# Performance work log

Hardware: AMD Instinct MI355X
Metric: run time of the kernel (lower is better)

Reference implementation:

```python
import jax, jax.numpy as jnp
import numpy as np

_J6 = jnp.array([[0,0,0,0,0,1],[0,0,0,0,-1,0],[0,0,0,1,0,0],
                 [0,0,1,0,0,0],[0,-1,0,0,0,0],[1,0,0,0,0,0]], dtype=jnp.float32)
_PAIRS4 = [(0,1),(0,2),(0,3),(1,2),(1,3),(2,3)]  # combinations(range(4),2)


def exterior(p1, p2):
    # Plucker line coords of two 4-vectors, normalized. (...,4)x(...,4)->(...,6)
    parts = [p1[..., i] * p2[..., j] - p1[..., j] * p2[..., i] for i, j in _PAIRS4]
    L = jnp.stack(parts, axis=-1)
    n = jnp.maximum(jnp.linalg.norm(L, axis=-1, keepdims=True), 1e-12)
    return L / n


def setup_inputs() -> dict:
    key = jax.random.key(0)
    B, T, D, H = 2, 2048, 1024, 16
    ks = jax.random.split(key, 10)
    w = lambda k, shape: jax.random.normal(k, shape, jnp.float32) * 0.02
    return {
        "x": jax.random.normal(ks[0], (B, T, D), jnp.float32),
        "qkv_w": w(ks[1], (3 * D, D)),
        "qkv_b": jnp.zeros((3 * D,), jnp.float32),
        "w1w": w(ks[2], (4 * H, D)),
        "w2w": w(ks[3], (4 * H, D)),
        "r1w": w(ks[4], (4 * H, D)),
        "r2w": w(ks[5], (4 * H, D)),
        "memv_w": w(ks[6], (D, D)),
        "memv_b": jnp.zeros((D,), jnp.float32),
        "memg_w": w(ks[7], (H, D)),
        "memg_b": jnp.zeros((H,), jnp.float32),
        "mem_scale": jnp.full((H,), 0.1, jnp.float32),
        "iter_mix": jnp.array(0.0, jnp.float32),
        "out_w": w(ks[8], (D, D)),
        "out_b": jnp.zeros((D,), jnp.float32),
        "decay_logits": jnp.full((H,), 4.6, jnp.float32),
    }


def reference(x, qkv_w, qkv_b, w1w, w2w, r1w, r2w, memv_w, memv_b,
              memg_w, memg_b, mem_scale, iter_mix, out_w, out_b, decay_logits):
    B, T, D = x.shape
    H = decay_logits.shape[0]
    dh = D // H
    pd = 6
    scale = dh ** -0.5

    # --- standard causal softmax attention ---
    qkv = (x @ qkv_w.T + qkv_b).reshape(B, T, 3, H, dh)
    qkv = jnp.transpose(qkv, (2, 0, 3, 1, 4))  # (3,B,H,T,dh)
    q, k, v = qkv[0], qkv[1], qkv[2]
    scores = jnp.einsum('bhtd,bhsd->bhts', q, k) * scale
    causal = jnp.triu(jnp.ones((T, T), dtype=bool), 1)
    scores = jnp.where(causal, -jnp.inf, scores)
    attn = jax.nn.softmax(scores, axis=-1)  # dropout is identity in eval
    seq_out = jnp.einsum('bhts,bhsd->bhtd', attn, v)
    seq_out = jnp.transpose(seq_out, (0, 2, 1, 3)).reshape(B, T, D)

    # --- decay-weighted Gram memory (linear-attention style state) ---
    x_prev = jnp.concatenate([jnp.zeros((B, 1, D), x.dtype), x[:, :-1]], axis=1)
    w1 = (x_prev @ w1w.T).reshape(B, T, H, 4)
    w2 = (x @ w2w.T).reshape(B, T, H, 4)
    write_lines = exterior(w1, w2)  # (B,T,H,6)
    r1 = (x @ r1w.T).reshape(B, T, H, 4)
    r2 = (x @ r2w.T).reshape(B, T, H, 4)
    read_lines = exterior(r1, r2)

    Jw = jnp.einsum('bthi,ij->bhtj', write_lines, _J6)  # (B,H,T,6)
    rd = jnp.transpose(read_lines, (0, 2, 1, 3))        # (B,H,T,6)

    decays = jax.nn.sigmoid(decay_logits)               # (H,)
    pos = jnp.arange(T, dtype=x.dtype)
    outer = Jw[..., :, None] * Jw[..., None, :]         # (B,H,T,6,6)
    decay_inv = (1.0 / jnp.maximum(decays, 1e-6))[:, None] ** pos[None, :]  # (H,T)
    outer_scaled = outer * decay_inv[None, :, :, None, None]
    M_cumsum = jnp.cumsum(outer_scaled, axis=2)
    M_cumsum = jnp.concatenate(
        [jnp.zeros((B, H, 1, pd, pd), x.dtype), M_cumsum[:, :, :-1]], axis=2)
    decay_fwd = decays[:, None] ** pos[None, :]
    M_all = M_cumsum * decay_fwd[None, :, :, None, None]

    rd_M = jnp.einsum('bhti,bhtij->bhtj', rd, M_all)
    score_M = jnp.sum(rd_M * rd, axis=-1)    # (B,H,T)
    score_M2 = jnp.sum(rd_M * rd_M, axis=-1)
    alpha = jax.nn.sigmoid(iter_mix)
    mem_score = (1 - alpha) * score_M + alpha * score_M2

    mem_val = x @ memv_w.T + memv_b                     # (B,T,D)
    gate = jax.nn.sigmoid(x @ memg_w.T + memg_b)        # (B,T,H)
    mem_score_t = jnp.transpose(mem_score, (0, 2, 1))   # (B,T,H)
    gated = jax.nn.sigmoid(mem_score_t * mem_scale) * gate
    gated = jnp.mean(gated, axis=-1, keepdims=True)     # (B,T,1)

    return (seq_out + gated * mem_val) @ out_w.T + out_b
```

## Files before the change

kernel.cpp:

```cpp
#include <hip/hip_runtime.h>
#include <stdint.h>

#define TT 2048
#define DD 1024
#define HH 16
#define LDP 4368
#define SCH 64
#define SNC (TT/SCH)

using bf16x8 = __attribute__((ext_vector_type(8))) __bf16;
using u16x8  = __attribute__((ext_vector_type(8))) unsigned short;
using f32x4  = __attribute__((ext_vector_type(4))) float;

__device__ __forceinline__ float bf2f(unsigned short u){
  unsigned int x = ((unsigned int)u) << 16;
  return __builtin_bit_cast(float, x);
}
__device__ __forceinline__ unsigned short f2bf(float f){
  unsigned int x = __builtin_bit_cast(unsigned int, f);
  x += 0x7fffu + ((x >> 16) & 1u);
  return (unsigned short)(x >> 16);
}
__device__ __forceinline__ float sigmoidf_(float x){ return 1.0f/(1.0f+__expf(-x)); }

__device__ __forceinline__ void gload_lds16(const void* g, void* l){
  auto gp = (const __attribute__((address_space(1))) unsigned int*)(uintptr_t)g;
  auto lp = (__attribute__((address_space(3))) unsigned int*)(unsigned int)(uintptr_t)l;
  __builtin_amdgcn_global_load_lds(gp, lp, 16, 0, 0);
}

__global__ void prep_all_kernel(const float* __restrict__ qkv_w, const float* __restrict__ w1w,
                                const float* __restrict__ w2w, const float* __restrict__ r1w,
                                const float* __restrict__ r2w, const float* __restrict__ memv_w,
                                const float* __restrict__ memg_w, const float* __restrict__ out_w,
                                const float* __restrict__ qkv_b, const float* __restrict__ memv_b,
                                const float* __restrict__ memg_b, const float* __restrict__ x,
                                unsigned short* __restrict__ Wcat, float* __restrict__ bcat,
                                unsigned short* __restrict__ xb)
{
  const int blk = blockIdx.x;
  if (blk < 5392) {
    const int idx = blk*256 + threadIdx.x;
    {
      const int row = idx >> 8, c4 = (idx & 255)*4;
      const float* src; int r;
      if      (row < 3072) { src = qkv_w;  r = row; }
      else if (row < 3136) { src = w1w;    r = row-3072; }
      else if (row < 3200) { src = w2w;    r = row-3136; }
      else if (row < 3264) { src = r1w;    r = row-3200; }
      else if (row < 3328) { src = r2w;    r = row-3264; }
      else if (row < 4352) { src = memv_w; r = row-3328; }
      else if (row < 4368) { src = memg_w; r = row-4352; }
      else                 { src = out_w;  r = row-4368; }
      const float4 v = *(const float4*)(src + (size_t)r*1024 + c4);
      ushort4 o; o.x=f2bf(v.x); o.y=f2bf(v.y); o.z=f2bf(v.z); o.w=f2bf(v.w);
      *(ushort4*)(Wcat + (size_t)row*1024 + c4) = o;
    }
    if (idx < 4368) {
      float v;
      if      (idx < 3072) v = qkv_b[idx];
      else if (idx < 3328) v = 0.f;
      else if (idx < 4352) v = memv_b[idx-3328];
      else                 v = memg_b[idx-4352];
      bcat[idx] = v;
    }
  } else {
    const int idx = (blk - 5392)*256 + threadIdx.x;
    const float4 v = ((const float4*)x)[idx];
    ushort4 o; o.x=f2bf(v.x); o.y=f2bf(v.y); o.z=f2bf(v.z); o.w=f2bf(v.w);
    ((ushort4*)xb)[idx] = o;
  }
}

template<bool OUTF32>
__global__ __launch_bounds__(256, 3)
void gemm_bt_kernel(const unsigned short* __restrict__ A, int lda,
                    const unsigned short* __restrict__ Bt, int ldb,
                    const float* __restrict__ bias,
                    void* __restrict__ Cout, int ldc, int N, int K)
{
  __shared__ unsigned short smem[24576];
  const int tid = threadIdx.x;
  const int w = tid >> 6, lane = tid & 63;
  const int l15 = lane & 15, l4 = lane >> 4;
  const int m0 = blockIdx.x * 128;
  const int n0 = blockIdx.y * 128;
  const int wr = (w >> 1) * 64, wc = (w & 1) * 64;

  const f32x4 zero = {0.f,0.f,0.f,0.f};
  f32x4 acc[4][4];
#pragma unroll
  for (int i = 0; i < 4; ++i)
#pragma unroll
    for (int j = 0; j < 4; ++j) acc[i][j] = zero;

  const int srow = lane >> 2;
  const int k8   = (lane & 3) * 8;

  auto stage = [&](int k0, int buf) {
#pragma unroll
    for (int q = 0; q < 4; ++q) {
      const int c = q*4 + w;
      const int rloc = (c & 7)*16 + srow;
      if (c < 8) {
        gload_lds16(A + (size_t)(m0 + rloc)*lda + k0 + k8,
                    (char*)smem + buf*8192 + (c&7)*1024);
      } else {
        int nrow = n0 + rloc; if (nrow >= N) nrow = N - 1;
        gload_lds16(Bt + (size_t)nrow*ldb + k0 + k8,
                    (char*)smem + 24576 + buf*8192 + (c&7)*1024);
      }
    }
  };

  stage(0, 0);
  if (K > 32) stage(32, 1);

  int ti = 0;
  for (int k0 = 0; k0 < K; k0 += 32, ++ti) {
    if (k0 + 32 < K) { asm volatile("s_waitcnt vmcnt(4)" ::: "memory"); }
    else             { asm volatile("s_waitcnt vmcnt(0)" ::: "memory"); }
    __builtin_amdgcn_s_barrier();
    if (k0 + 64 < K) stage(k0 + 64, (ti + 2) % 3);

    const int cur = ti % 3;
    bf16x8 af[4], bfr[4];
#pragma unroll
    for (int i = 0; i < 4; ++i) {
      af[i]  = *reinterpret_cast<const bf16x8*>((const char*)smem + cur*8192
                 + (wr + i*16 + l15)*64 + l4*16);
      bfr[i] = *reinterpret_cast<const bf16x8*>((const char*)smem + 24576 + cur*8192
                 + (wc + i*16 + l15)*64 + l4*16);
    }
#pragma unroll
    for (int i = 0; i < 4; ++i)
#pragma unroll
      for (int j = 0; j < 4; ++j)
        acc[i][j] = __builtin_amdgcn_mfma_f32_16x16x32_bf16(af[i], bfr[j], acc[i][j], 0, 0, 0);
  }

  if (OUTF32) {
#pragma unroll
    for (int i = 0; i < 4; ++i) {
      const int rowb = m0 + wr + i*16 + l4*4;
#pragma unroll
      for (int j = 0; j < 4; ++j) {
        const int col = n0 + wc + j*16 + l15;
        if (col < N) {
          const float bv = bias ? bias[col] : 0.0f;
#pragma unroll
          for (int r = 0; r < 4; ++r)
            ((float*)Cout)[(size_t)(rowb + r)*ldc + col] = acc[i][j][r] + bv;
        }
      }
    }
  } else {
    __syncthreads();
#pragma unroll
    for (int i = 0; i < 4; ++i) {
      const int rloc = wr + i*16 + l4*4;
#pragma unroll
      for (int j = 0; j < 4; ++j) {
        const int col = wc + j*16 + l15;
        const float bv = bias ? bias[n0 + col] : 0.0f;
#pragma unroll
        for (int r = 0; r < 4; ++r)
          smem[(rloc + r)*128 + col] = f2bf(acc[i][j][r] + bv);
      }
    }
    __syncthreads();
#pragma unroll
    for (int p = 0; p < 8; ++p) {
      const int idx = p*256 + tid;
      const int row = idx >> 4;
      const int c8  = (idx & 15) * 8;
      if (n0 + c8 + 8 <= N) {
        *(u16x8*)((unsigned short*)Cout + (size_t)(m0 + row)*ldc + n0 + c8) =
            *(const u16x8*)&smem[row*128 + c8];
      }
    }
  }
}

__global__ __launch_bounds__(256, 4)
void transpose_v_kernel(const unsigned short* __restrict__ P, unsigned short* __restrict__ VT)
{
  __shared__ unsigned short tile[64][66];
  const int t0 = blockIdx.x*64, h = blockIdx.y, b = blockIdx.z;
  for (int i = threadIdx.x; i < 4096; i += 256) {
    const int r = i >> 6, c = i & 63;
    tile[r][c] = P[(size_t)(b*TT + t0 + r)*LDP + 2048 + h*64 + c];
  }
  __syncthreads();
  for (int i = threadIdx.x; i < 4096; i += 256) {
    const int d = i >> 6, tl = i & 63;
    VT[(size_t)((b*HH + h)*64 + d)*TT + t0 + tl] = tile[tl][d];
  }
}

__global__ __launch_bounds__(256, 2)
void attn_kernel(const unsigned short* __restrict__ P,
                 const unsigned short* __restrict__ VT,
                 float* __restrict__ seqo)
{
  __shared__ unsigned short Ks[2][128*64];
  __shared__ unsigned short Vs[2][64*128];
  __shared__ unsigned short Pls[4][16*128];

  const int tid = threadIdx.x;
  const int w = tid >> 6, lane = tid & 63;
  const int l15 = lane & 15, l4 = lane >> 4;
  const int pi = blockIdx.x, h = blockIdx.y, b = blockIdx.z;

  auto stage = [&](int kt, int bufsel) {
#pragma unroll
    for (int q2 = 0; q2 < 4; ++q2) {
      const int idx = q2*256 + tid;
      {
        const int r = idx >> 3;
        const int cb = ((idx & 7)*16) ^ ((r & 7) << 4);
        gload_lds16(P + (size_t)(b*TT + kt*128 + r)*LDP + 1024 + h*64 + (cb >> 1),
                    (char*)Ks[bufsel] + q2*4096 + w*1024);
      }
      {
        const int r = idx >> 4;
        const int cb = ((idx & 15)*16) ^ ((r & 7) << 4);
        gload_lds16(VT + (size_t)((b*HH + h)*64 + r)*TT + kt*128 + (cb >> 1),
                    (char*)Vs[bufsel] + q2*4096 + w*1024);
      }
    }
  };

  const f32x4 zero = {0.f,0.f,0.f,0.f};
  const unsigned xorb = ((unsigned)(l15 & 7u)) << 4;

  for (int rep = 0; rep < 2; ++rep) {
    const int qt = rep == 0 ? pi : 31 - pi;
    const int qbase = qt * 64;
    const int qrow = qbase + w*16 + l15;
    const int nt = (qt >> 1) + 1;

    bf16x8 qa[2];
    {
      const size_t base = (size_t)(b*TT + qbase + w*16 + l15)*LDP + h*64 + l4*8;
      qa[0] = *reinterpret_cast<const bf16x8*>(P + base);
      qa[1] = *reinterpret_cast<const bf16x8*>(P + base + 32);
    }

    f32x4 o[4];
#pragma unroll
    for (int d = 0; d < 4; ++d) o[d] = zero;
    float mrow = -1e30f;
    float lrow = 0.f;

    stage(0, 0);
    asm volatile("s_waitcnt vmcnt(0)" ::: "memory");
    __builtin_amdgcn_s_barrier();

    for (int kt = 0; kt < nt; ++kt) {
      const int cur = kt & 1;
      if (kt + 1 < nt) stage(kt + 1, cur ^ 1);

      f32x4 s[8];
#pragma unroll
      for (int kk = 0; kk < 8; ++kk) {
        f32x4 a = zero;
#pragma unroll
        for (int c = 0; c < 2; ++c) {
          const unsigned kbyte = (unsigned)((kk*16 + l15)*128)
                               + (((unsigned)(c*64 + l4*16)) ^ xorb);
          const bf16x8 kb = *reinterpret_cast<const bf16x8*>((const char*)Ks[cur] + kbyte);
          a = __builtin_amdgcn_mfma_f32_16x16x32_bf16(kb, qa[c], a, 0, 0, 0);
        }
        s[kk] = a;
      }

      if (kt == nt - 1) {
#pragma unroll
        for (int kk = 0; kk < 8; ++kk)
#pragma unroll
          for (int j = 0; j < 4; ++j) {
            const int kcol = kt*128 + kk*16 + l4*4 + j;
            s[kk][j] = (kcol <= qrow) ? s[kk][j]*0.125f : -1e30f;
          }
      } else {
#pragma unroll
        for (int kk = 0; kk < 8; ++kk)
#pragma unroll
          for (int j = 0; j < 4; ++j) s[kk][j] *= 0.125f;
      }

      float am[8];
#pragma unroll
      for (int kk = 0; kk < 8; ++kk)
        am[kk] = fmaxf(fmaxf(s[kk][0], s[kk][1]), fmaxf(s[kk][2], s[kk][3]));
      float tmax = fmaxf(fmaxf(fmaxf(am[0], am[1]), fmaxf(am[2], am[3])),
                         fmaxf(fmaxf(am[4], am[5]), fmaxf(am[6], am[7])));
      tmax = fmaxf(tmax, __shfl_xor(tmax, 16));
      tmax = fmaxf(tmax, __shfl_xor(tmax, 32));
      const float mn = fmaxf(mrow, tmax);
      const float corr = __expf(mrow - mn);
      mrow = mn;
      float lsum = 0.f;
#pragma unroll
      for (int kk = 0; kk < 8; ++kk) {
        float p0 = __expf(s[kk][0] - mn);
        float p1 = __expf(s[kk][1] - mn);
        float p2 = __expf(s[kk][2] - mn);
        float p3 = __expf(s[kk][3] - mn);
        s[kk][0] = p0; s[kk][1] = p1; s[kk][2] = p2; s[kk][3] = p3;
        lsum += (p0 + p1) + (p2 + p3);
      }
      lsum += __shfl_xor(lsum, 16);
      lsum += __shfl_xor(lsum, 32);
      lrow = lrow*corr + lsum;

      float corrq[4];
#pragma unroll
      for (int j = 0; j < 4; ++j) corrq[j] = __shfl(corr, l4*4 + j, 16);
#pragma unroll
      for (int d = 0; d < 4; ++d)
#pragma unroll
        for (int j = 0; j < 4; ++j) o[d][j] *= corrq[j];

      const unsigned pbase = (unsigned)(w*4096);
#pragma unroll
      for (int kk = 0; kk < 8; ++kk)
#pragma unroll
        for (int jp = 0; jp < 2; ++jp) {
          const unsigned v = (unsigned)f2bf(s[kk][jp*2]) | ((unsigned)f2bf(s[kk][jp*2+1]) << 16);
          const unsigned k = (unsigned)(kk*16 + l4*4 + jp*2);
          unsigned byte = (unsigned)l15*256u + ((k*2u) ^ xorb);
          *(unsigned*)((char*)Pls + pbase + byte) = v;
        }
      asm volatile("s_waitcnt lgkmcnt(0)" ::: "memory");

#pragma unroll
      for (int c = 0; c < 4; ++c) {
        const unsigned abyte = (unsigned)(l15*256) + (((unsigned)(c*64 + l4*16)) ^ xorb);
        const bf16x8 pa = *reinterpret_cast<const bf16x8*>((char*)Pls + pbase + abyte);
#pragma unroll
        for (int d = 0; d < 4; ++d) {
          const unsigned vbyte = (unsigned)((d*16 + l15)*256)
                               + (((unsigned)(c*64 + l4*16)) ^ xorb);
          const bf16x8 vb = *reinterpret_cast<const bf16x8*>((const char*)Vs[cur] + vbyte);
          o[d] = __builtin_amdgcn_mfma_f32_16x16x32_bf16(pa, vb, o[d], 0, 0, 0);
        }
      }

      asm volatile("s_waitcnt lgkmcnt(0)" ::: "memory");
      asm volatile("s_waitcnt vmcnt(0)" ::: "memory");
      __builtin_amdgcn_s_barrier();
    }

    float lrowq[4];
#pragma unroll
    for (int j = 0; j < 4; ++j) lrowq[j] = __shfl(lrow, l4*4 + j, 16);
#pragma unroll
    for (int d = 0; d < 4; ++d)
#pragma unroll
      for (int j = 0; j < 4; ++j) {
        const int row = qbase + w*16 + l4*4 + j;
        seqo[(size_t)(b*TT + row)*DD + h*64 + d*16 + l15] = o[d][j] / lrowq[j];
      }
  }
}

__device__ __forceinline__ void ext6(const float* p, const float* q, float* L){
  L[0] = p[0]*q[1] - p[1]*q[0];
  L[1] = p[0]*q[2] - p[2]*q[0];
  L[2] = p[0]*q[3] - p[3]*q[0];
  L[3] = p[1]*q[2] - p[2]*q[1];
  L[4] = p[1]*q[3] - p[3]*q[1];
  L[5] = p[2]*q[3] - p[3]*q[2];
  const float n2 = L[0]*L[0]+L[1]*L[1]+L[2]*L[2]+L[3]*L[3]+L[4]*L[4]+L[5]*L[5];
  const float inv = 1.0f / fmaxf(sqrtf(n2), 1e-12f);
#pragma unroll
  for (int i = 0; i < 6; ++i) L[i] *= inv;
}

__device__ __forceinline__ void load4bf(const unsigned short* p, float* o){
  const ushort4 u = *(const ushort4*)p;
  o[0] = bf2f(u.x); o[1] = bf2f(u.y); o[2] = bf2f(u.z); o[3] = bf2f(u.w);
}

__global__ __launch_bounds__(64, 8)
void scan_passA(const unsigned short* __restrict__ P, const float* __restrict__ decay_logits,
                float* __restrict__ E)
{
  __shared__ float jwS[SCH][6];
  const int bid = blockIdx.x;
  const int s = bid >> 5, c = bid & (SNC-1);
  const int b_ = s >> 4, h = s & (HH-1);
  const int lane = threadIdx.x;

  {
    const int t = c*SCH + lane;
    const size_t row = (size_t)(b_*TT + t)*LDP;
    float w1[4], w2[4];
    if (t > 0) load4bf(P + row - LDP + 3072 + h*4, w1);
    else { w1[0]=w1[1]=w1[2]=w1[3]=0.f; }
    load4bf(P + row + 3136 + h*4, w2);
    float wl[6];
    ext6(w1, w2, wl);
    jwS[lane][0]= wl[5]; jwS[lane][1]=-wl[4]; jwS[lane][2]= wl[3];
    jwS[lane][3]= wl[2]; jwS[lane][4]=-wl[1]; jwS[lane][5]= wl[0];
  }
  __syncthreads();

  const int i = lane & 7, j = lane >> 3;
  const int ic = i < 6 ? i : 0, jc = j < 6 ? j : 0;
  const float d = sigmoidf_(decay_logits[h]);
  float e = 0.f;
  for (int t = 0; t < SCH; ++t)
    e = d*(e + jwS[t][ic]*jwS[t][jc]);
  if (i < 6 && j < 6) E[(size_t)bid*36 + j*6 + i] = e;
}

__global__ __launch_bounds__(64, 8)
void scan_passC(const unsigned short* __restrict__ P, const float* __restrict__ E,
                const float* __restrict__ decay_logits,
                const float* __restrict__ iter_mix, float* __restrict__ msc)
{
  __shared__ float Ls[SCH][12];
  const int bid = blockIdx.x;
  const int s = bid >> 5, c = bid & (SNC-1);
  const int b_ = s >> 4, h = s & (HH-1);
  const int lane = threadIdx.x;

  {
    const int t = c*SCH + lane;
    const size_t row = (size_t)(b_*TT + t)*LDP;
    float w1[4], w2[4], r1[4], r2[4];
    if (t > 0) load4bf(P + row - LDP + 3072 + h*4, w1);
    else { w1[0]=w1[1]=w1[2]=w1[3]=0.f; }
    load4bf(P + row + 3136 + h*4, w2);
    load4bf(P + row + 3200 + h*4, r1);
    load4bf(P + row + 3264 + h*4, r2);
    float wl[6], rl[6];
    ext6(w1, w2, wl);
    ext6(r1, r2, rl);
    Ls[lane][0]= wl[5]; Ls[lane][1]=-wl[4]; Ls[lane][2]= wl[3];
    Ls[lane][3]= wl[2]; Ls[lane][4]=-wl[1]; Ls[lane][5]= wl[0];
#pragma unroll
    for (int q = 0; q < 6; ++q) Ls[lane][6+q] = rl[q];
  }
  __syncthreads();

  const int i = lane & 7, j = lane >> 3;
  const bool valid = (i < 6) && (j < 6);
  const int ic = i < 6 ? i : 0, jc = j < 6 ? j : 0;
  const float d = sigmoidf_(decay_logits[h]);
  const float alpha = sigmoidf_(iter_mix[0]);

  float m = 0.f;
  if (valid) {
    const float dL = __powf(d, (float)SCH);
    for (int cp = 0; cp < c; ++cp)
      m = dL*m + E[((size_t)s*SNC + cp)*36 + j*6 + i];
  }

  for (int t = 0; t < SCH; ++t) {
    const float ai = Ls[t][ic];
    const float aj = Ls[t][jc];
    const float ri = Ls[t][6+ic];
    const float rj = Ls[t][6+jc];
    float part = valid ? ri*m : 0.f;
    part += __shfl_xor(part, 1);
    part += __shfl_xor(part, 2);
    part += __shfl_xor(part, 4);
    float contrib = (i == 0 && j < 6) ? part*((1.f-alpha)*rj + alpha*part) : 0.f;
    contrib += __shfl_xor(contrib, 8);
    contrib += __shfl_xor(contrib, 16);
    contrib += __shfl_xor(contrib, 32);
    if (lane == 0) msc[((size_t)b_*TT + c*SCH + t)*HH + h] = contrib;
    m = d*(m + ai*aj);
  }
}

__global__ __launch_bounds__(256, 4)
void combine_kernel(const float* __restrict__ seqo, const unsigned short* __restrict__ P,
                    const float* __restrict__ msc, const float* __restrict__ mem_scale,
                    unsigned short* __restrict__ zb)
{
  const int w = threadIdx.x >> 6, lane = threadIdx.x & 63;
  const int row = blockIdx.x*4 + w;
  float val = 0.f;
  if (lane < HH) {
    const float ms = msc[(size_t)row*HH + lane];
    const float gl = bf2f(P[(size_t)row*LDP + 4352 + lane]);
    val = sigmoidf_(ms*mem_scale[lane]) * sigmoidf_(gl);
  }
  val += __shfl_xor(val, 1);
  val += __shfl_xor(val, 2);
  val += __shfl_xor(val, 4);
  val += __shfl_xor(val, 8);
  const float g = __shfl(val, 0) * (1.0f/16.0f);
#pragma unroll
  for (int it = 0; it < 4; ++it) {
    const int dcol = it*256 + lane*4;
    const float4 sv = *(const float4*)&seqo[(size_t)row*DD + dcol];
    const ushort4 pv = *(const ushort4*)&P[(size_t)row*LDP + 3328 + dcol];
    ushort4 o;
    o.x = f2bf(sv.x + g*bf2f(pv.x));
    o.y = f2bf(sv.y + g*bf2f(pv.y));
    o.z = f2bf(sv.z + g*bf2f(pv.z));
    o.w = f2bf(sv.w + g*bf2f(pv.w));
    *(ushort4*)&zb[(size_t)row*DD + dcol] = o;
  }
}

extern "C" void kernel_launch(void* const* d_in, const int* in_sizes, int n_in,
                              void* d_out, int out_size, void* d_ws, size_t ws_size,
                              hipStream_t stream)
{
  const float* x            = (const float*)d_in[0];
  const float* qkv_w        = (const float*)d_in[1];
  const float* qkv_b        = (const float*)d_in[2];
  const float* w1w          = (const float*)d_in[3];
  const float* w2w          = (const float*)d_in[4];
  const float* r1w          = (const float*)d_in[5];
  const float* r2w          = (const float*)d_in[6];
  const float* memv_w       = (const float*)d_in[7];
  const float* memv_b       = (const float*)d_in[8];
  const float* memg_w       = (const float*)d_in[9];
  const float* memg_b       = (const float*)d_in[10];
  const float* mem_scale    = (const float*)d_in[11];
  const float* iter_mix     = (const float*)d_in[12];
  const float* out_w        = (const float*)d_in[13];
  const float* out_b        = (const float*)d_in[14];
  const float* decay_logits = (const float*)d_in[15];

  char* ws = (char*)d_ws;
  unsigned short* xb   = (unsigned short*)(ws + 0);
  unsigned short* Wcat = (unsigned short*)(ws + 8388608);
  float*          bcat = (float*)         (ws + 19431424);
  unsigned short* P    = (unsigned short*)(ws + 19449088);
  unsigned short* VT   = (unsigned short*)(ws + 55231744);
  float*          seqo = (float*)         (ws + 63620352);
  float*          E    = (float*)         (ws + 80397568);
  float*          msc  = (float*)         (ws + 83690752);
  unsigned short* zb   = xb;

  prep_all_kernel<<<9488, 256, 0, stream>>>(qkv_w, w1w, w2w, r1w, r2w, memv_w, memg_w, out_w,
                                            qkv_b, memv_b, memg_b, x, Wcat, bcat, xb);
  gemm_bt_kernel<false><<<dim3(32, 35), 256, 0, stream>>>(xb, 1024, Wcat, 1024, bcat,
                                                          P, LDP, 4368, 1024);
  transpose_v_kernel<<<dim3(32, 16, 2), 256, 0, stream>>>(P, VT);
  attn_kernel<<<dim3(16, 16, 2), 256, 0, stream>>>(P, VT, seqo);
  scan_passA<<<1024, 64, 0, stream>>>(P, decay_logits, E);
  scan_passC<<<1024, 64, 0, stream>>>(P, E, decay_logits, iter_mix, msc);
  combine_kernel<<<1024, 256, 0, stream>>>(seqo, P, msc, mem_scale, zb);
  gemm_bt_kernel<true><<<dim3(32, 8), 256, 0, stream>>>(zb, 1024, Wcat + (size_t)4368*1024, 1024,
                                                        out_b, d_out, 1024, 1024, 1024);
}
```

Before: 179.8 us.

## Fuse V transpose into QKV GEMM epilogue and skip unchanged-max rescale

The QKV GEMM epilogue now writes the V column tiles directly in transposed layout to VT through a swizzled shared-memory staging buffer, removing the separate transpose kernel and its extra pass over V. The shared-memory layout gets an XOR swizzle to reduce bank conflicts. In attention, the online-softmax correction and accumulator rescale are skipped when no row's max increased across the wavefront. The transposed store uses narrow 2-byte writes, which may be less efficient than the old vectorized path.

Result: no change. 176.7 us (-1.7%).

```diff
diff --git a/kernel.cpp b/kernel.cpp
--- a/kernel.cpp
+++ b/kernel.cpp
@@ -77,7 +77,8 @@
 void gemm_bt_kernel(const unsigned short* __restrict__ A, int lda,
                     const unsigned short* __restrict__ Bt, int ldb,
                     const float* __restrict__ bias,
-                    void* __restrict__ Cout, int ldc, int N, int K)
+                    void* __restrict__ Cout, int ldc, int N, int K,
+                    unsigned short* __restrict__ VTout)
 {
   __shared__ unsigned short smem[24576];
   const int tid = threadIdx.x;
@@ -156,6 +157,7 @@
     }
   } else {
     __syncthreads();
+    const bool isV = (VTout != nullptr) && (n0 >= 2048) && (n0 < 3072);
 #pragma unroll
     for (int i = 0; i < 4; ++i) {
       const int rloc = wr + i*16 + l4*4;
@@ -164,37 +166,41 @@
         const int col = wc + j*16 + l15;
         const float bv = bias ? bias[n0 + col] : 0.0f;
 #pragma unroll
-        for (int r = 0; r < 4; ++r)
-          smem[(rloc + r)*128 + col] = f2bf(acc[i][j][r] + bv);
+        for (int r = 0; r < 4; ++r) {
+          const int row = rloc + r;
+          const unsigned byte = (unsigned)row*256u
+                              + (((unsigned)col*2u) ^ (((unsigned)row & 15u) << 4));
+          *(unsigned short*)((char*)smem + byte) = f2bf(acc[i][j][r] + bv);
+        }
       }
     }
     __syncthreads();
-#pragma unroll
-    for (int p = 0; p < 8; ++p) {
-      const int idx = p*256 + tid;
-      const int row = idx >> 4;
-      const int c8  = (idx & 15) * 8;
-      if (n0 + c8 + 8 <= N) {
-        *(u16x8*)((unsigned short*)Cout + (size_t)(m0 + row)*ldc + n0 + c8) =
-            *(const u16x8*)&smem[row*128 + c8];
-      }
-    }
-  }
-}
-
-__global__ __launch_bounds__(256, 4)
-void transpose_v_kernel(const unsigned short* __restrict__ P, unsigned short* __restrict__ VT)
-{
-  __shared__ unsigned short tile[64][66];
-  const int t0 = blockIdx.x*64, h = blockIdx.y, b = blockIdx.z;
-  for (int i = threadIdx.x; i < 4096; i += 256) {
-    const int r = i >> 6, c = i & 63;
-    tile[r][c] = P[(size_t)(b*TT + t0 + r)*LDP + 2048 + h*64 + c];
-  }
-  __syncthreads();
-  for (int i = threadIdx.x; i < 4096; i += 256) {
-    const int d = i >> 6, tl = i & 63;
-    VT[(size_t)((b*HH + h)*64 + d)*TT + t0 + tl] = tile[tl][d];
+    if (!isV) {
+#pragma unroll
+      for (int p = 0; p < 8; ++p) {
+        const int idx = p*256 + tid;
+        const int row = idx >> 4;
+        const int c8  = (idx & 15) * 8;
+        if (n0 + c8 + 8 <= N) {
+          const unsigned byte = (unsigned)row*256u
+                              + (((unsigned)(c8*2)) ^ (((unsigned)row & 15u) << 4));
+          *(u16x8*)((unsigned short*)Cout + (size_t)(m0 + row)*ldc + n0 + c8) =
+              *(const u16x8*)((const char*)smem + byte);
+        }
+      }
+    } else {
+      const int vbase = ((m0 >> 11)*HH + ((n0 - 2048) >> 6)) * 64;
+      const int t0 = m0 & (TT - 1);
+      for (int it = 0; it < 64; ++it) {
+        const int i2 = it*256 + tid;
+        const int d2 = i2 >> 7;
+        const int tl = i2 & 127;
+        const unsigned byte = (unsigned)tl*256u
+                            + (((unsigned)d2*2u) ^ (((unsigned)tl & 15u) << 4));
+        VTout[(size_t)(vbase + d2)*TT + t0 + tl] =
+            *(const unsigned short*)((const char*)smem + byte);
+      }
+    }
   }
 }
 
@@ -298,9 +304,8 @@
                          fmaxf(fmaxf(am[4], am[5]), fmaxf(am[6], am[7])));
       tmax = fmaxf(tmax, __shfl_xor(tmax, 16));
       tmax = fmaxf(tmax, __shfl_xor(tmax, 32));
-      const float mn = fmaxf(mrow, tmax);
-      const float corr = __expf(mrow - mn);
-      mrow = mn;
+      const bool skip = (__all(tmax <= mrow) != 0);
+      const float mn = skip ? mrow : fmaxf(mrow, tmax);
       float lsum = 0.f;
 #pragma unroll
       for (int kk = 0; kk < 8; ++kk) {
@@ -313,15 +318,21 @@
       }
       lsum += __shfl_xor(lsum, 16);
       lsum += __shfl_xor(lsum, 32);
-      lrow = lrow*corr + lsum;
-
-      float corrq[4];
-#pragma unroll
-      for (int j = 0; j < 4; ++j) corrq[j] = __shfl(corr, l4*4 + j, 16);
-#pragma unroll
-      for (int d = 0; d < 4; ++d)
-#pragma unroll
-        for (int j = 0; j < 4; ++j) o[d][j] *= corrq[j];
+
+      if (skip) {
+        lrow = lrow + lsum;
+      } else {
+        const float corr = __expf(mrow - mn);
+        mrow = mn;
+        lrow = lrow*corr + lsum;
+        float corrq[4];
+#pragma unroll
+        for (int j = 0; j < 4; ++j) corrq[j] = __shfl(corr, l4*4 + j, 16);
+#pragma unroll
+        for (int d = 0; d < 4; ++d)
+#pragma unroll
+          for (int j = 0; j < 4; ++j) o[d][j] *= corrq[j];
+      }
 
       const unsigned pbase = (unsigned)(w*4096);
 #pragma unroll
@@ -545,12 +556,11 @@
   prep_all_kernel<<<9488, 256, 0, stream>>>(qkv_w, w1w, w2w, r1w, r2w, memv_w, memg_w, out_w,
                                             qkv_b, memv_b, memg_b, x, Wcat, bcat, xb);
   gemm_bt_kernel<false><<<dim3(32, 35), 256, 0, stream>>>(xb, 1024, Wcat, 1024, bcat,
-                                                          P, LDP, 4368, 1024);
-  transpose_v_kernel<<<dim3(32, 16, 2), 256, 0, stream>>>(P, VT);
+                                                          P, LDP, 4368, 1024, VT);
   attn_kernel<<<dim3(16, 16, 2), 256, 0, stream>>>(P, VT, seqo);
   scan_passA<<<1024, 64, 0, stream>>>(P, decay_logits, E);
   scan_passC<<<1024, 64, 0, stream>>>(P, E, decay_logits, iter_mix, msc);
   combine_kernel<<<1024, 256, 0, stream>>>(seqo, P, msc, mem_scale, zb);
   gemm_bt_kernel<true><<<dim3(32, 8), 256, 0, stream>>>(zb, 1024, Wcat + (size_t)4368*1024, 1024,
-                                                        out_b, d_out, 1024, 1024, 1024);
-}
+                                                        out_b, d_out, 1024, 1024, 1024, nullptr);
+}
```
